# Performance work log

Measured on AMD Instinct MI355X. Metric: run time of the kernel, lower is better.

Reference implementation:

```python
import jax, jax.numpy as jnp
import numpy as np

K = 3  # kernel_size


def conv2d_same(x, w, b):
    # x: NHWC, w: HWIO
    y = jax.lax.conv_general_dilated(
        x, w, window_strides=(1, 1), padding='SAME',
        dimension_numbers=('NHWC', 'HWIO', 'NHWC'))
    return y + b


def setup_inputs() -> dict:
    key = jax.random.key(0)
    k0, k1, k2 = jax.random.split(key, 3)
    B, H, Wd, C, F = 8, 128, 128, 64, 128
    x = jax.random.normal(k0, (B, H, Wd, C), jnp.float32)
    # offset conv: small random weights (zeros in original init -> degenerate),
    # scaled down so offsets stay in a realistic few-pixel range
    W_off = jax.random.normal(k1, (K, K, C, 2 * K * K), jnp.float32) * 0.01
    b_off = jnp.zeros((2 * K * K,), jnp.float32)
    fan_in = K * K * K * K * C
    W = jax.random.normal(k2, (K, K, K * K * C, F), jnp.float32) / np.float32(np.sqrt(fan_in))
    b = jnp.zeros((F,), jnp.float32)
    return {"x": x, "W_off": W_off, "b_off": b_off, "W": W, "b": b}


def reference(x, W_off, b_off, W, b):
    B, H, Wd, C = x.shape
    KK = K * K
    # predicted per-pixel, per-tap (dx, dy) offsets
    offsets = conv2d_same(x, W_off, b_off).reshape(B, H, Wd, KK, 2)

    # base pixel grid, stacked as (x, y) like the original
    gy, gx = jnp.meshgrid(jnp.arange(H, dtype=jnp.float32),
                          jnp.arange(Wd, dtype=jnp.float32), indexing='ij')
    grid = jnp.stack([gx, gy], axis=-1)[None, :, :, None, :]  # (1,H,W,1,2)

    # kernel tap grid, 'xy' meshgrid like tf.meshgrid default
    off = (K - 1) / 2.0
    lin = jnp.linspace(-off, off, K).astype(jnp.float32)
    kx, ky = jnp.meshgrid(lin, lin)
    kgrid = jnp.stack([kx, ky], axis=-1).reshape(1, 1, 1, KK, 2)

    loc = grid + kgrid + offsets  # (B,H,W,KK,2)
    lx = jnp.clip(loc[..., 0], 0.0, Wd - 1.0)
    ly = jnp.clip(loc[..., 1], 0.0, H - 1.0)

    x0 = jnp.clip(jnp.floor(lx), 0.0, Wd - 1.0)
    x1 = jnp.clip(jnp.floor(lx) + 1.0, 0.0, Wd - 1.0)
    y0 = jnp.clip(jnp.floor(ly), 0.0, H - 1.0)
    y1 = jnp.clip(jnp.floor(ly) + 1.0, 0.0, H - 1.0)

    # weights computed from the CLIPPED corner coords, as in the original
    wa = (x1 - lx) * (y1 - ly)
    wb = (x1 - lx) * (ly - y0)
    wc = (lx - x0) * (y1 - ly)
    wd = (lx - x0) * (ly - y0)

    x0i, x1i = x0.astype(jnp.int32), x1.astype(jnp.int32)
    y0i, y1i = y0.astype(jnp.int32), y1.astype(jnp.int32)

    xf = x.reshape(B, H * Wd, C)

    def gather(yi, xi):
        idx = (yi * Wd + xi).reshape(B, -1)           # (B, H*W*KK)
        g = jax.vmap(lambda f, i: f[i])(xf, idx)      # (B, P, C)
        return g.reshape(B, H, Wd, KK, C)

    Ia = gather(y0i, x0i)
    Ib = gather(y1i, x0i)
    Ic = gather(y0i, x1i)
    Id = gather(y1i, x1i)

    sampled = (wa[..., None] * Ia + wb[..., None] * Ib
               + wc[..., None] * Ic + wd[..., None] * Id)
    sampled = sampled.reshape(B, H, Wd, KK * C)
    return conv2d_same(sampled, W, b)
```

## Files before the change

kernel.cpp:

```cpp
#include <hip/hip_runtime.h>
#include <hip/hip_bf16.h>

#define B_   8
#define H_   128
#define W_   128
#define C_   64
#define F_   128
#define KDIM 5184
#define BHW_ 131072

#define TH   8
#define TW   16
#define HY   10
#define HX   18
#define NPX  180

#define STILE 0
#define BT    11520
#define PARMW 36096
#define PARMO 37536
#define LDSSZ 38976

typedef __bf16 bf16x8 __attribute__((ext_vector_type(8)));
typedef float  f32x4  __attribute__((ext_vector_type(4)));

__device__ __forceinline__ unsigned short f2bf(float f) {
  unsigned int u = __float_as_uint(f);
  unsigned int r = (u + 0x7fffu + ((u >> 16) & 1u)) >> 16;
  return (unsigned short)r;
}

__global__ __launch_bounds__(256) void woff_prep_kernel(
    const float* __restrict__ Woff, unsigned short* __restrict__ WbHi,
    unsigned short* __restrict__ WbLo) {
  int u = blockIdx.x * 256 + threadIdx.x;
  if (u >= 18432) return;
  int j  = u & 7;
  int kq = (u >> 3) & 3;
  int n  = (u >> 5) & 15;
  int nt = (u >> 9) & 1;
  int tc = u >> 10;
  int tap = tc >> 1, kch = tc & 1;
  int o = nt * 16 + n;
  int c = kch * 32 + kq * 8 + j;
  float val = 0.f;
  if (o < 18) val = Woff[(tap * 64 + c) * 18 + o];
  unsigned short h = f2bf(val);
  float hf = __uint_as_float((unsigned)h << 16);
  WbHi[u] = h;
  WbLo[u] = f2bf(val - hf);
}

__global__ __launch_bounds__(256, 3) void offs_mfma_kernel(
    const float* __restrict__ x, const unsigned short* __restrict__ WbHi,
    const unsigned short* __restrict__ WbLo, const float* __restrict__ boff,
    float* __restrict__ offsP) {
  __shared__ __align__(16) short lds[26112];
  const int tid = threadIdx.x, lane = tid & 63, w = tid >> 6;
  const int bid = blockIdx.x;
  const int b  = bid >> 7;
  const int t  = bid & 127;
  const int r4 = t >> 2, cq = t & 3;
  const int gy0 = r4 * 4, gx0 = cq * 32;
  const float* xb = x + (size_t)b * (H_ * W_ * C_);

#pragma unroll
  for (int it = 0; it < 7; ++it) {
    int u = it * 256 + tid;
    if (u < 1632) {
      int p = u >> 3, j = u & 7;
      int rowi = p / 34, coli = p - rowi * 34;
      int gy = gy0 - 1 + rowi, gx = gx0 - 1 + coli;
      union { __bf16 h[8]; uint4 v; } hi, lo;
      if ((unsigned)gy < (unsigned)H_ && (unsigned)gx < (unsigned)W_) {
        const float* src = xb + (((gy << 7) + gx) << 6) + j * 8;
        float4 v0 = ((const float4*)src)[0], v1 = ((const float4*)src)[1];
        float f[8] = {v0.x, v0.y, v0.z, v0.w, v1.x, v1.y, v1.z, v1.w};
#pragma unroll
        for (int e = 0; e < 8; ++e) {
          __bf16 h16 = (__bf16)f[e];
          hi.h[e] = h16;
          lo.h[e] = (__bf16)(f[e] - (float)h16);
        }
      } else {
        hi.v = make_uint4(0, 0, 0, 0);
        lo.v = hi.v;
      }
      int a = p * 64 + ((j ^ (coli & 7)) * 8);
      *(uint4*)&lds[a] = hi.v;
      *(uint4*)&lds[13056 + a] = lo.v;
    }
  }
  __syncthreads();

  const int l15 = lane & 15, kq = lane >> 4;
  const int bbase = (l15 * 4 + kq) * 8;
  f32x4 acc[2][2] = {};

#pragma unroll
  for (int ky = 0; ky < 3; ++ky) {
#pragma unroll
    for (int kx = 0; kx < 3; ++kx) {
      const int tap = ky * 3 + kx;
#pragma unroll
      for (int kch = 0; kch < 2; ++kch) {
        const int tc = tap * 2 + kch;
        bf16x8 bh0 = *(const bf16x8*)&WbHi[tc * 1024 + bbase];
        bf16x8 bh1 = *(const bf16x8*)&WbHi[tc * 1024 + 512 + bbase];
        bf16x8 bl0 = *(const bf16x8*)&WbLo[tc * 1024 + bbase];
        bf16x8 bl1 = *(const bf16x8*)&WbLo[tc * 1024 + 512 + bbase];
#pragma unroll
        for (int mt = 0; mt < 2; ++mt) {
          int coli = mt * 16 + l15 + kx;
          int px = (w + ky) * 34 + coli;
          int a = px * 64 + (((kch * 4 + kq) ^ (coli & 7)) * 8);
          bf16x8 ah = *(const bf16x8*)&lds[a];
          bf16x8 al = *(const bf16x8*)&lds[13056 + a];
          acc[mt][0] = __builtin_amdgcn_mfma_f32_16x16x32_bf16(ah, bh0, acc[mt][0], 0, 0, 0);
          acc[mt][0] = __builtin_amdgcn_mfma_f32_16x16x32_bf16(al, bh0, acc[mt][0], 0, 0, 0);
          acc[mt][0] = __builtin_amdgcn_mfma_f32_16x16x32_bf16(ah, bl0, acc[mt][0], 0, 0, 0);
          acc[mt][1] = __builtin_amdgcn_mfma_f32_16x16x32_bf16(ah, bh1, acc[mt][1], 0, 0, 0);
          acc[mt][1] = __builtin_amdgcn_mfma_f32_16x16x32_bf16(al, bh1, acc[mt][1], 0, 0, 0);
          acc[mt][1] = __builtin_amdgcn_mfma_f32_16x16x32_bf16(ah, bl1, acc[mt][1], 0, 0, 0);
        }
      }
    }
  }

  __syncthreads();
  float* accbuf = (float*)lds;
  float bv0 = boff[l15];
  float bv1 = boff[min(16 + l15, 17)];
#pragma unroll
  for (int mt = 0; mt < 2; ++mt)
#pragma unroll
    for (int r = 0; r < 4; ++r) {
      int px = mt * 16 + kq * 4 + r;
      accbuf[(w * 32 + px) * 19 + l15] = acc[mt][0][r] + bv0;
      if (l15 < 2)
        accbuf[(w * 32 + px) * 19 + 16 + l15] = acc[mt][1][r] + bv1;
    }
  __syncthreads();
  const int lane32 = tid & 31, tpi = tid >> 5;
#pragma unroll
  for (int v = 0; v < 9; ++v) {
    int u = v * 8 + tpi;
    int o = u >> 2, w2 = u & 3;
    float val = accbuf[(w2 * 32 + lane32) * 19 + o];
    offsP[(size_t)o * BHW_ + (size_t)b * 16384 + (gy0 + w2) * 128 + gx0 + lane32] = val;
  }
}

__global__ __launch_bounds__(256) void wt_prep_kernel(
    const float* __restrict__ Wf, unsigned short* __restrict__ Wt) {
  __shared__ float Wl[64][65];
  const int tid = threadIdx.x;
  const int kk0 = (blockIdx.x % 81) * 64;
  const int f0  = (blockIdx.x / 81) * 64;
  for (int i = tid; i < 4096; i += 256) {
    int kk = i >> 6, f = i & 63;
    Wl[kk][f] = Wf[(size_t)(kk0 + kk) * F_ + f0 + f];
  }
  __syncthreads();
  for (int i = tid; i < 4096; i += 256) {
    int f = i >> 6, kk = i & 63;
    Wt[(size_t)(f0 + f) * KDIM + kk0 + kk] = f2bf(Wl[kk][f]);
  }
}

#define STAGE_SUB(tt, tp2, fsv, bufv)                                          \
  do {                                                                         \
    _Pragma("unroll")                                                          \
    for (int li_ = 0; li_ < 4; ++li_) {                                        \
      int f_ = wn + (fsv) * 32 + li_ * 8 + rig;                                \
      const short* src_ = (const short*)Wt + (size_t)f_ * KDIM +               \
                          (tp2) * 576 + (tt) * 64 + ((sub ^ rig) * 8);         \
      __builtin_amdgcn_global_load_lds(                                        \
          (const __attribute__((address_space(1))) void*)src_,                 \
          (__attribute__((address_space(3))) void*)                            \
              &lds[wbase + (bufv) * 2048 + li_ * 512],                         \
          16, 0, 0);                                                           \
    }                                                                          \
  } while (0)

__global__ __launch_bounds__(256, 2) void fused_kernel(
    const float* __restrict__ x, const float* __restrict__ offsP,
    const unsigned short* __restrict__ Wt, const float* __restrict__ bias,
    float* __restrict__ out) {
  __shared__ __align__(16) short lds[LDSSZ];
  const int tid  = threadIdx.x;
  const int lane = tid & 63;
  const int wv   = tid >> 6;
  const int gr   = (blockIdx.x & 7) * 128 + (blockIdx.x >> 3);
  const int b    = gr >> 7;
  const int tile = gr & 127;
  const int ty   = tile >> 3, tx = tile & 7;
  const int gy0  = ty * TH, gx0 = tx * TW;
  const float* xb = x + (size_t)b * (H_ * W_ * C_);

  const int l15  = lane & 15, quad = lane >> 4;
  const int sub  = lane & 7,  rig  = lane >> 3;
  const int wn   = (wv & 1) * 64;
  const int wbase = BT + wv * 6144;

  f32x4 acc[4][4] = {};

  int p0[4];
#pragma unroll
  for (int i = 0; i < 4; ++i) p0[i] = ((wv >> 1) * 4 + i) * HX + l15;
  int bo2[2][2];
#pragma unroll
  for (int ks = 0; ks < 2; ++ks)
#pragma unroll
    for (int j2 = 0; j2 < 2; ++j2)
      bo2[ks][j2] = (16 * j2 + l15) * 64 + (((ks * 4 + quad) ^ (l15 & 7)) * 8);

  const int s_py = tid / HX, s_px = tid - s_py * HX;

  for (int t = 0; t < 9; ++t) {
    __syncthreads();
    if (tid < NPX) {
      int gy = gy0 + s_py - 1, gx = gx0 + s_px - 1;
      float wa = 0.f, wb = 0.f, wc = 0.f, wd = 0.f;
      int oA = 0, oB = 0, oC = 0, oD = 0;
      if ((unsigned)gy < (unsigned)H_ && (unsigned)gx < (unsigned)W_) {
        int pix = (b * H_ + gy) * W_ + gx;
        float offx = offsP[(size_t)(2 * t) * BHW_ + pix];
        float offy = offsP[(size_t)(2 * t + 1) * BHW_ + pix];
        float lx = (float)gx + (float)(t % 3 - 1) + offx;
        float ly = (float)gy + (float)(t / 3 - 1) + offy;
        lx = fminf(fmaxf(lx, 0.f), 127.f);
        ly = fminf(fmaxf(ly, 0.f), 127.f);
        float fx = floorf(lx), fy = floorf(ly);
        float x0c = fminf(fmaxf(fx, 0.f), 127.f);
        float x1c = fminf(fmaxf(fx + 1.f, 0.f), 127.f);
        float y0c = fminf(fmaxf(fy, 0.f), 127.f);
        float y1c = fminf(fmaxf(fy + 1.f, 0.f), 127.f);
        wa = (x1c - lx) * (y1c - ly);
        wb = (x1c - lx) * (ly - y0c);
        wc = (lx - x0c) * (y1c - ly);
        wd = (lx - x0c) * (ly - y0c);
        int ix0 = (int)x0c, ix1 = (int)x1c, iy0 = (int)y0c, iy1 = (int)y1c;
        oA = (iy0 * W_ + ix0) * C_;
        oB = (iy1 * W_ + ix0) * C_;
        oC = (iy0 * W_ + ix1) * C_;
        oD = (iy1 * W_ + ix1) * C_;
      }
      ((float4*)&lds[PARMW])[tid] = make_float4(wa, wb, wc, wd);
      ((int4*)&lds[PARMO])[tid]  = make_int4(oA | (s_px << 20), oB, oC, oD);
    }
    __syncthreads();
    STAGE_SUB(t, 0, 0, 0);
    STAGE_SUB(t, 0, 1, 1);
#pragma unroll
    for (int it = 0; it < 6; ++it) {
      int u = it * 256 + tid;
      if (u < NPX * 8) {
        int p = u >> 3, j = u & 7;
        float4 wv4 = ((const float4*)&lds[PARMW])[p];
        int4   ov4 = ((const int4*)&lds[PARMO])[p];
        int pxl = ov4.x >> 20;
        const float* pa = xb + (ov4.x & 0xFFFFF) + j * 8;
        const float* pb = xb + ov4.y + j * 8;
        const float* pc = xb + ov4.z + j * 8;
        const float* pd = xb + ov4.w + j * 8;
        float4 A0 = ((const float4*)pa)[0], A1 = ((const float4*)pa)[1];
        float4 B0 = ((const float4*)pb)[0], B1 = ((const float4*)pb)[1];
        float4 C0 = ((const float4*)pc)[0], C1 = ((const float4*)pc)[1];
        float4 D0 = ((const float4*)pd)[0], D1 = ((const float4*)pd)[1];
        union { __bf16 h[8]; uint4 v; } uu;
        uu.h[0] = (__bf16)(wv4.x * A0.x + wv4.y * B0.x + wv4.z * C0.x + wv4.w * D0.x);
        uu.h[1] = (__bf16)(wv4.x * A0.y + wv4.y * B0.y + wv4.z * C0.y + wv4.w * D0.y);
        uu.h[2] = (__bf16)(wv4.x * A0.z + wv4.y * B0.z + wv4.z * C0.z + wv4.w * D0.z);
        uu.h[3] = (__bf16)(wv4.x * A0.w + wv4.y * B0.w + wv4.z * C0.w + wv4.w * D0.w);
        uu.h[4] = (__bf16)(wv4.x * A1.x + wv4.y * B1.x + wv4.z * C1.x + wv4.w * D1.x);
        uu.h[5] = (__bf16)(wv4.x * A1.y + wv4.y * B1.y + wv4.z * C1.y + wv4.w * D1.y);
        uu.h[6] = (__bf16)(wv4.x * A1.z + wv4.y * B1.z + wv4.z * C1.z + wv4.w * D1.z);
        uu.h[7] = (__bf16)(wv4.x * A1.w + wv4.y * B1.w + wv4.z * C1.w + wv4.w * D1.w);
        *(uint4*)&lds[STILE + p * 64 + ((j ^ (pxl & 7)) * 8)] = uu.v;
      }
    }
    __syncthreads();

#pragma unroll
    for (int tap2 = 0; tap2 < 9; ++tap2) {
      const int g = tap2 / 3, c3 = tap2 % 3;
      const int t1 = (l15 + c3) & 7;
      bf16x8 af[2][4];
#pragma unroll
      for (int ks = 0; ks < 2; ++ks)
#pragma unroll
        for (int i = 0; i < 4; ++i)
          af[ks][i] = *(const bf16x8*)&lds[(p0[i] + g * HX + c3) * 64 +
                                           (((ks * 4 + quad) ^ t1) * 8)];
#pragma unroll
      for (int fs = 0; fs < 2; ++fs) {
        const int s = tap2 * 2 + fs;
        if (s <= 15) {
          STAGE_SUB(t, (s + 2) >> 1, (s + 2) & 1, (s + 2) % 3);
        }
        if (s < 16)        asm volatile("s_waitcnt vmcnt(8)" ::: "memory");
        else if (s == 16)  asm volatile("s_waitcnt vmcnt(4)" ::: "memory");
        else               asm volatile("s_waitcnt vmcnt(0)" ::: "memory");
        __builtin_amdgcn_sched_barrier(0);
        const int cb = wbase + (s % 3) * 2048;
        __builtin_amdgcn_s_setprio(1);
#pragma unroll
        for (int ks = 0; ks < 2; ++ks) {
          bf16x8 b0 = *(const bf16x8*)&lds[cb + bo2[ks][0]];
          bf16x8 b1 = *(const bf16x8*)&lds[cb + bo2[ks][1]];
#pragma unroll
          for (int i = 0; i < 4; ++i) {
            acc[i][fs * 2 + 0] = __builtin_amdgcn_mfma_f32_16x16x32_bf16(
                af[ks][i], b0, acc[i][fs * 2 + 0], 0, 0, 0);
            acc[i][fs * 2 + 1] = __builtin_amdgcn_mfma_f32_16x16x32_bf16(
                af[ks][i], b1, acc[i][fs * 2 + 1], 0, 0, 0);
          }
        }
        __builtin_amdgcn_s_setprio(0);
      }
    }
  }

  float bj[4];
#pragma unroll
  for (int j = 0; j < 4; ++j) bj[j] = bias[wn + 16 * j + l15];
#pragma unroll
  for (int i = 0; i < 4; ++i) {
    int gy = gy0 + (wv >> 1) * 4 + i;
#pragma unroll
    for (int r = 0; r < 4; ++r) {
      int gx = gx0 + quad * 4 + r;
      float* rp = out + ((size_t)((b * H_ + gy) * W_ + gx)) * F_;
#pragma unroll
      for (int j = 0; j < 4; ++j)
        rp[wn + 16 * j + l15] = acc[i][j][r] + bj[j];
    }
  }
}

extern "C" void kernel_launch(void* const* d_in, const int* in_sizes, int n_in,
                              void* d_out, int out_size, void* d_ws, size_t ws_size,
                              hipStream_t stream) {
  (void)in_sizes; (void)n_in; (void)out_size; (void)ws_size;
  const float* x    = (const float*)d_in[0];
  const float* Woff = (const float*)d_in[1];
  const float* boff = (const float*)d_in[2];
  const float* Wf   = (const float*)d_in[3];
  const float* bias = (const float*)d_in[4];
  float* out = (float*)d_out;

  char* ws = (char*)d_ws;
  size_t off_bytes = (size_t)18 * BHW_ * 4;
  size_t p1 = (off_bytes + 255) & ~(size_t)255;
  size_t wt_bytes = (size_t)F_ * KDIM * 2;
  float*          offsP = (float*)ws;
  unsigned short* Wt    = (unsigned short*)(ws + p1);
  unsigned short* WbHi  = (unsigned short*)(ws + p1 + wt_bytes);
  unsigned short* WbLo  = WbHi + 18432;

  woff_prep_kernel<<<72, 256, 0, stream>>>(Woff, WbHi, WbLo);
  offs_mfma_kernel<<<1024, 256, 0, stream>>>(x, WbHi, WbLo, boff, offsP);
  wt_prep_kernel<<<162, 256, 0, stream>>>(Wf, Wt);
  fused_kernel<<<1024, 256, 0, stream>>>(x, offsP, Wt, bias, out);
}
```

Baseline: 312.6 us.

## Warp-specialize fused kernel: producer waves sample, consumer waves run MFMA

The block grows to 512 threads. Four producer waves compute the bilinear-sampled tile for the next tap into a double-buffered LDS region, while four consumer waves run the MFMA GEMM on the current tap and prefetch the next tap's weights. The per-tap parameter staging in LDS is gone: producers compute offsets and weights inline per chunk. This is meant to overlap the gather and sampling latency with the matrix math. In exchange it uses more LDS and twice the threads at occupancy 2, and producers recompute the sampling parameters 8 times per pixel.

```diff
diff --git a/kernel.cpp b/kernel.cpp
--- a/kernel.cpp
+++ b/kernel.cpp
@@ -15,11 +15,9 @@
 #define HX   18
 #define NPX  180
 
-#define STILE 0
-#define BT    11520
-#define PARMW 36096
-#define PARMO 37536
-#define LDSSZ 38976
+#define SBUF  11520
+#define BT    23040
+#define LDSSZ 47616
 
 typedef __bf16 bf16x8 __attribute__((ext_vector_type(8)));
 typedef float  f32x4  __attribute__((ext_vector_type(4)));
@@ -183,7 +181,7 @@
     }                                                                          \
   } while (0)
 
-__global__ __launch_bounds__(256, 2) void fused_kernel(
+__global__ __launch_bounds__(512, 2) void fused_kernel(
     const float* __restrict__ x, const float* __restrict__ offsP,
     const unsigned short* __restrict__ Wt, const float* __restrict__ bias,
     float* __restrict__ out) {
@@ -200,14 +198,15 @@
 
   const int l15  = lane & 15, quad = lane >> 4;
   const int sub  = lane & 7,  rig  = lane >> 3;
-  const int wn   = (wv & 1) * 64;
-  const int wbase = BT + wv * 6144;
+  const int wvc  = wv & 3;
+  const int wn   = (wvc & 1) * 64;
+  const int wbase = BT + wvc * 6144;
 
   f32x4 acc[4][4] = {};
 
   int p0[4];
 #pragma unroll
-  for (int i = 0; i < 4; ++i) p0[i] = ((wv >> 1) * 4 + i) * HX + l15;
+  for (int i = 0; i < 4; ++i) p0[i] = ((wvc >> 1) * 4 + i) * HX + l15;
   int bo2[2][2];
 #pragma unroll
   for (int ks = 0; ks < 2; ++ks)
@@ -215,126 +214,138 @@
     for (int j2 = 0; j2 < 2; ++j2)
       bo2[ks][j2] = (16 * j2 + l15) * 64 + (((ks * 4 + quad) ^ (l15 & 7)) * 8);
 
-  const int s_py = tid / HX, s_px = tid - s_py * HX;
-
-  for (int t = 0; t < 9; ++t) {
-    __syncthreads();
-    if (tid < NPX) {
-      int gy = gy0 + s_py - 1, gx = gx0 + s_px - 1;
-      float wa = 0.f, wb = 0.f, wc = 0.f, wd = 0.f;
-      int oA = 0, oB = 0, oC = 0, oD = 0;
-      if ((unsigned)gy < (unsigned)H_ && (unsigned)gx < (unsigned)W_) {
-        int pix = (b * H_ + gy) * W_ + gx;
-        float offx = offsP[(size_t)(2 * t) * BHW_ + pix];
-        float offy = offsP[(size_t)(2 * t + 1) * BHW_ + pix];
-        float lx = (float)gx + (float)(t % 3 - 1) + offx;
-        float ly = (float)gy + (float)(t / 3 - 1) + offy;
-        lx = fminf(fmaxf(lx, 0.f), 127.f);
-        ly = fminf(fmaxf(ly, 0.f), 127.f);
-        float fx = floorf(lx), fy = floorf(ly);
-        float x0c = fminf(fmaxf(fx, 0.f), 127.f);
-        float x1c = fminf(fmaxf(fx + 1.f, 0.f), 127.f);
-        float y0c = fminf(fmaxf(fy, 0.f), 127.f);
-        float y1c = fminf(fmaxf(fy + 1.f, 0.f), 127.f);
-        wa = (x1c - lx) * (y1c - ly);
-        wb = (x1c - lx) * (ly - y0c);
-        wc = (lx - x0c) * (y1c - ly);
-        wd = (lx - x0c) * (ly - y0c);
-        int ix0 = (int)x0c, ix1 = (int)x1c, iy0 = (int)y0c, iy1 = (int)y1c;
-        oA = (iy0 * W_ + ix0) * C_;
-        oB = (iy1 * W_ + ix0) * C_;
-        oC = (iy0 * W_ + ix1) * C_;
-        oD = (iy1 * W_ + ix1) * C_;
-      }
-      ((float4*)&lds[PARMW])[tid] = make_float4(wa, wb, wc, wd);
-      ((int4*)&lds[PARMO])[tid]  = make_int4(oA | (s_px << 20), oB, oC, oD);
-    }
-    __syncthreads();
-    STAGE_SUB(t, 0, 0, 0);
-    STAGE_SUB(t, 0, 1, 1);
+  auto S2FULL = [&](int tt, int pb) {
+    const int sbw = pb * SBUF;
+    const float kxo = (float)(tt % 3 - 1);
+    const float kyo = (float)(tt / 3 - 1);
 #pragma unroll
     for (int it = 0; it < 6; ++it) {
       int u = it * 256 + tid;
       if (u < NPX * 8) {
         int p = u >> 3, j = u & 7;
-        float4 wv4 = ((const float4*)&lds[PARMW])[p];
-        int4   ov4 = ((const int4*)&lds[PARMO])[p];
-        int pxl = ov4.x >> 20;
-        const float* pa = xb + (ov4.x & 0xFFFFF) + j * 8;
-        const float* pb = xb + ov4.y + j * 8;
-        const float* pc = xb + ov4.z + j * 8;
-        const float* pd = xb + ov4.w + j * 8;
-        float4 A0 = ((const float4*)pa)[0], A1 = ((const float4*)pa)[1];
-        float4 B0 = ((const float4*)pb)[0], B1 = ((const float4*)pb)[1];
-        float4 C0 = ((const float4*)pc)[0], C1 = ((const float4*)pc)[1];
-        float4 D0 = ((const float4*)pd)[0], D1 = ((const float4*)pd)[1];
-        union { __bf16 h[8]; uint4 v; } uu;
-        uu.h[0] = (__bf16)(wv4.x * A0.x + wv4.y * B0.x + wv4.z * C0.x + wv4.w * D0.x);
-        uu.h[1] = (__bf16)(wv4.x * A0.y + wv4.y * B0.y + wv4.z * C0.y + wv4.w * D0.y);
-        uu.h[2] = (__bf16)(wv4.x * A0.z + wv4.y * B0.z + wv4.z * C0.z + wv4.w * D0.z);
-        uu.h[3] = (__bf16)(wv4.x * A0.w + wv4.y * B0.w + wv4.z * C0.w + wv4.w * D0.w);
-        uu.h[4] = (__bf16)(wv4.x * A1.x + wv4.y * B1.x + wv4.z * C1.x + wv4.w * D1.x);
-        uu.h[5] = (__bf16)(wv4.x * A1.y + wv4.y * B1.y + wv4.z * C1.y + wv4.w * D1.y);
-        uu.h[6] = (__bf16)(wv4.x * A1.z + wv4.y * B1.z + wv4.z * C1.z + wv4.w * D1.z);
-        uu.h[7] = (__bf16)(wv4.x * A1.w + wv4.y * B1.w + wv4.z * C1.w + wv4.w * D1.w);
-        *(uint4*)&lds[STILE + p * 64 + ((j ^ (pxl & 7)) * 8)] = uu.v;
+        int rowi = (p * 456) >> 13;
+        int coli = p - rowi * 18;
+        int gy = gy0 + rowi - 1, gx = gx0 + coli - 1;
+        uint4 sv = make_uint4(0, 0, 0, 0);
+        if ((unsigned)gy < (unsigned)H_ && (unsigned)gx < (unsigned)W_) {
+          int pix = (b * H_ + gy) * W_ + gx;
+          float offx = offsP[(size_t)(2 * tt) * BHW_ + pix];
+          float offy = offsP[(size_t)(2 * tt + 1) * BHW_ + pix];
+          float lx = (float)gx + kxo + offx;
+          float ly = (float)gy + kyo + offy;
+          lx = fminf(fmaxf(lx, 0.f), 127.f);
+          ly = fminf(fmaxf(ly, 0.f), 127.f);
+          float fx = floorf(lx), fy = floorf(ly);
+          float x0c = fminf(fmaxf(fx, 0.f), 127.f);
+          float x1c = fminf(fmaxf(fx + 1.f, 0.f), 127.f);
+          float y0c = fminf(fmaxf(fy, 0.f), 127.f);
+          float y1c = fminf(fmaxf(fy + 1.f, 0.f), 127.f);
+          float wa = (x1c - lx) * (y1c - ly);
+          float wb = (x1c - lx) * (ly - y0c);
+          float wc = (lx - x0c) * (y1c - ly);
+          float wd = (lx - x0c) * (ly - y0c);
+          int ix0 = (int)x0c, ix1 = (int)x1c, iy0 = (int)y0c, iy1 = (int)y1c;
+          const float* pa = xb + (iy0 * W_ + ix0) * C_ + j * 8;
+          const float* pb2 = xb + (iy1 * W_ + ix0) * C_ + j * 8;
+          const float* pc = xb + (iy0 * W_ + ix1) * C_ + j * 8;
+          const float* pd = xb + (iy1 * W_ + ix1) * C_ + j * 8;
+          float4 A0 = ((const float4*)pa)[0], A1 = ((const float4*)pa)[1];
+          float4 B0 = ((const float4*)pb2)[0], B1 = ((const float4*)pb2)[1];
+          float4 C0 = ((const float4*)pc)[0], C1 = ((const float4*)pc)[1];
+          float4 D0 = ((const float4*)pd)[0], D1 = ((const float4*)pd)[1];
+          union { __bf16 h[8]; uint4 v; } uu;
+          uu.h[0] = (__bf16)(wa * A0.x + wb * B0.x + wc * C0.x + wd * D0.x);
+          uu.h[1] = (__bf16)(wa * A0.y + wb * B0.y + wc * C0.y + wd * D0.y);
+          uu.h[2] = (__bf16)(wa * A0.z + wb * B0.z + wc * C0.z + wd * D0.z);
+          uu.h[3] = (__bf16)(wa * A0.w + wb * B0.w + wc * C0.w + wd * D0.w);
+          uu.h[4] = (__bf16)(wa * A1.x + wb * B1.x + wc * C1.x + wd * D1.x);
+          uu.h[5] = (__bf16)(wa * A1.y + wb * B1.y + wc * C1.y + wd * D1.y);
+          uu.h[6] = (__bf16)(wa * A1.z + wb * B1.z + wc * C1.z + wd * D1.z);
+          uu.h[7] = (__bf16)(wa * A1.w + wb * B1.w + wc * C1.w + wd * D1.w);
+          sv = uu.v;
+        }
+        *(uint4*)&lds[sbw + p * 64 + ((j ^ (coli & 7)) * 8)] = sv;
+      }
+    }
+  };
+
+  if (wv < 4) {
+    S2FULL(0, 0);
+  } else {
+    STAGE_SUB(0, 0, 0, 0);
+    STAGE_SUB(0, 0, 1, 1);
+  }
+  __syncthreads();
+
+  for (int t = 0; t < 9; ++t) {
+    if (wv < 4) {
+      if (t < 8) S2FULL(t + 1, (t + 1) & 1);
+    } else {
+      const int sb = (t & 1) * SBUF;
+#pragma unroll
+      for (int tap2 = 0; tap2 < 9; ++tap2) {
+        const int g = tap2 / 3, c3 = tap2 % 3;
+        const int t1 = (l15 + c3) & 7;
+        bf16x8 af[2][4];
+#pragma unroll
+        for (int ks = 0; ks < 2; ++ks)
+#pragma unroll
+          for (int i = 0; i < 4; ++i)
+            af[ks][i] = *(const bf16x8*)&lds[sb + (p0[i] + g * HX + c3) * 64 +
+                                             (((ks * 4 + quad) ^ t1) * 8)];
+#pragma unroll
+        for (int fs = 0; fs < 2; ++fs) {
+          const int s = tap2 * 2 + fs;
+          if (s <= 15) {
+            STAGE_SUB(t, (s + 2) >> 1, (s + 2) & 1, (s + 2) % 3);
+            if (s == 0) asm volatile("s_waitcnt vmcnt(4)" ::: "memory");
+            else        asm volatile("s_waitcnt vmcnt(8)" ::: "memory");
+          } else {
+            if (t < 8) {
+              STAGE_SUB(t + 1, 0, s - 16, (s + 2) % 3);
+              asm volatile("s_waitcnt vmcnt(8)" ::: "memory");
+            } else {
+              if (s == 16) asm volatile("s_waitcnt vmcnt(4)" ::: "memory");
+              else         asm volatile("s_waitcnt vmcnt(0)" ::: "memory");
+            }
+          }
+          __builtin_amdgcn_sched_barrier(0);
+          const int cb = wbase + (s % 3) * 2048;
+          __builtin_amdgcn_s_setprio(1);
+#pragma unroll
+          for (int ks = 0; ks < 2; ++ks) {
+            bf16x8 b0 = *(const bf16x8*)&lds[cb + bo2[ks][0]];
+            bf16x8 b1 = *(const bf16x8*)&lds[cb + bo2[ks][1]];
+#pragma unroll
+            for (int i = 0; i < 4; ++i) {
+              acc[i][fs * 2 + 0] = __builtin_amdgcn_mfma_f32_16x16x32_bf16(
+                  af[ks][i], b0, acc[i][fs * 2 + 0], 0, 0, 0);
+              acc[i][fs * 2 + 1] = __builtin_amdgcn_mfma_f32_16x16x32_bf16(
+                  af[ks][i], b1, acc[i][fs * 2 + 1], 0, 0, 0);
+            }
+          }
+          __builtin_amdgcn_s_setprio(0);
+        }
       }
     }
     __syncthreads();
-
-#pragma unroll
-    for (int tap2 = 0; tap2 < 9; ++tap2) {
-      const int g = tap2 / 3, c3 = tap2 % 3;
-      const int t1 = (l15 + c3) & 7;
-      bf16x8 af[2][4];
-#pragma unroll
-      for (int ks = 0; ks < 2; ++ks)
-#pragma unroll
-        for (int i = 0; i < 4; ++i)
-          af[ks][i] = *(const bf16x8*)&lds[(p0[i] + g * HX + c3) * 64 +
-                                           (((ks * 4 + quad) ^ t1) * 8)];
-#pragma unroll
-      for (int fs = 0; fs < 2; ++fs) {
-        const int s = tap2 * 2 + fs;
-        if (s <= 15) {
-          STAGE_SUB(t, (s + 2) >> 1, (s + 2) & 1, (s + 2) % 3);
-        }
-        if (s < 16)        asm volatile("s_waitcnt vmcnt(8)" ::: "memory");
-        else if (s == 16)  asm volatile("s_waitcnt vmcnt(4)" ::: "memory");
-        else               asm volatile("s_waitcnt vmcnt(0)" ::: "memory");
-        __builtin_amdgcn_sched_barrier(0);
-        const int cb = wbase + (s % 3) * 2048;
-        __builtin_amdgcn_s_setprio(1);
-#pragma unroll
-        for (int ks = 0; ks < 2; ++ks) {
-          bf16x8 b0 = *(const bf16x8*)&lds[cb + bo2[ks][0]];
-          bf16x8 b1 = *(const bf16x8*)&lds[cb + bo2[ks][1]];
-#pragma unroll
-          for (int i = 0; i < 4; ++i) {
-            acc[i][fs * 2 + 0] = __builtin_amdgcn_mfma_f32_16x16x32_bf16(
-                af[ks][i], b0, acc[i][fs * 2 + 0], 0, 0, 0);
-            acc[i][fs * 2 + 1] = __builtin_amdgcn_mfma_f32_16x16x32_bf16(
-                af[ks][i], b1, acc[i][fs * 2 + 1], 0, 0, 0);
-          }
-        }
-        __builtin_amdgcn_s_setprio(0);
-      }
-    }
-  }
-
-  float bj[4];
-#pragma unroll
-  for (int j = 0; j < 4; ++j) bj[j] = bias[wn + 16 * j + l15];
-#pragma unroll
-  for (int i = 0; i < 4; ++i) {
-    int gy = gy0 + (wv >> 1) * 4 + i;
-#pragma unroll
-    for (int r = 0; r < 4; ++r) {
-      int gx = gx0 + quad * 4 + r;
-      float* rp = out + ((size_t)((b * H_ + gy) * W_ + gx)) * F_;
-#pragma unroll
-      for (int j = 0; j < 4; ++j)
-        rp[wn + 16 * j + l15] = acc[i][j][r] + bj[j];
+  }
+
+  if (wv >= 4) {
+    float bj[4];
+#pragma unroll
+    for (int j = 0; j < 4; ++j) bj[j] = bias[wn + 16 * j + l15];
+#pragma unroll
+    for (int i = 0; i < 4; ++i) {
+      int gy = gy0 + (wvc >> 1) * 4 + i;
+#pragma unroll
+      for (int r = 0; r < 4; ++r) {
+        int gx = gx0 + quad * 4 + r;
+        float* rp = out + ((size_t)((b * H_ + gy) * W_ + gx)) * F_;
+#pragma unroll
+        for (int j = 0; j < 4; ++j)
+          rp[wn + 16 * j + l15] = acc[i][j][r] + bj[j];
+      }
     }
   }
 }
@@ -362,5 +373,5 @@
   woff_prep_kernel<<<72, 256, 0, stream>>>(Woff, WbHi, WbLo);
   offs_mfma_kernel<<<1024, 256, 0, stream>>>(x, WbHi, WbLo, boff, offsP);
   wt_prep_kernel<<<162, 256, 0, stream>>>(Wf, Wt);
-  fused_kernel<<<1024, 256, 0, stream>>>(x, offsP, Wt, bias, out);
-}
+  fused_kernel<<<1024, 512, 0, stream>>>(x, offsP, Wt, bias, out);
+}
```

After: 321.2 us. 2.7% more time.
